# Kernel optimization log

Hardware: AMD Instinct MI355X
Metric: run time of the kernel (lower is better)

## Reference

```python
import jax, jax.numpy as jnp
import numpy as np

N_NODES = 50000
N_EDGES = 800000
IN_DIM = 128
HEADS1, D1 = 4, 16   # hidden_dim // 4 = 16, concat -> 64
HID = HEADS1 * D1    # 64
OUT_DIM = 40
NEG_SLOPE = 0.2      # PyG GATConv default


def setup_inputs() -> dict:
    key = jax.random.key(0)
    ks = jax.random.split(key, 11)
    x = jax.random.normal(ks[0], (N_NODES, IN_DIM), dtype=jnp.float32)
    edge_index = jax.random.randint(ks[1], (2, N_EDGES), 0, N_NODES)
    s1 = 1.0 / np.sqrt(IN_DIM)
    s2 = 1.0 / np.sqrt(HID)
    return {
        "x": x,
        "edge_index": edge_index,
        "W1": jax.random.normal(ks[2], (IN_DIM, HEADS1 * D1), dtype=jnp.float32) * s1,
        "a_src1": jax.random.normal(ks[3], (HEADS1, D1), dtype=jnp.float32) * s2,
        "a_dst1": jax.random.normal(ks[4], (HEADS1, D1), dtype=jnp.float32) * s2,
        "b1": jnp.zeros((HID,), dtype=jnp.float32),
        "W2": jax.random.normal(ks[5], (HID, OUT_DIM), dtype=jnp.float32) * s2,
        "a_src2": jax.random.normal(ks[6], (1, OUT_DIM), dtype=jnp.float32) * s2,
        "a_dst2": jax.random.normal(ks[7], (1, OUT_DIM), dtype=jnp.float32) * s2,
        "b2": jnp.zeros((OUT_DIM,), dtype=jnp.float32),
    }


def gat_conv(x, src, dst, W, a_src, a_dst, b, heads, d, n_nodes):
    # linear projection, split into heads: [N, H, d]
    h = (x @ W).reshape(n_nodes, heads, d)
    # per-node attention logits: [N, H]
    alpha_src = jnp.einsum("nhd,hd->nh", h, a_src)
    alpha_dst = jnp.einsum("nhd,hd->nh", h, a_dst)
    # edge attention coefficients
    e = jax.nn.leaky_relu(alpha_src[src] + alpha_dst[dst], NEG_SLOPE)  # [E, H]
    # segment softmax over incoming edges of each destination node
    e_max = jax.ops.segment_max(e, dst, num_segments=n_nodes)
    e_max = jnp.where(jnp.isfinite(e_max), e_max, 0.0)
    e_exp = jnp.exp(e - e_max[dst])
    denom = jax.ops.segment_sum(e_exp, dst, num_segments=n_nodes)
    alpha = e_exp / (denom[dst] + 1e-16)  # [E, H]
    # weighted scatter-aggregate of source messages
    out = jax.ops.segment_sum(h[src] * alpha[..., None], dst, num_segments=n_nodes)
    return out.reshape(n_nodes, heads * d) + b


def reference(x, edge_index, W1, a_src1, a_dst1, b1, W2, a_src2, a_dst2, b2):
    n = x.shape[0]
    # PyG GATConv add_self_loops=True
    loop = jnp.arange(n, dtype=edge_index.dtype)
    src = jnp.concatenate([edge_index[0], loop])
    dst = jnp.concatenate([edge_index[1], loop])
    h = jax.nn.relu(gat_conv(x, src, dst, W1, a_src1, a_dst1, b1, HEADS1, D1, n))
    # dropout is identity in eval mode
    h = gat_conv(h, src, dst, W2, a_src2, a_dst2, b2, 1, OUT_DIM, n)
    return jax.nn.log_softmax(h, axis=1)
```

## Files before the change

### kernel.cpp

```cpp
#include <hip/hip_runtime.h>
#include <hip/hip_fp16.h>
#include <math.h>

#define NN    50000
#define NE0   800000
#define NE    850000
#define INDIM 128
#define HID   64
#define OUTD  40

#define NB    391
#define BSH   7
#define BCAP  3072

typedef unsigned short u16;

__global__ __launch_bounds__(256) void k_bin(const int* __restrict__ ei,
                                             int* __restrict__ bcur,
                                             unsigned int* __restrict__ epack) {
    __shared__ int lh[NB];
    __shared__ int lbase[NB];
    __shared__ unsigned ebuf[3328];
    const int tid = threadIdx.x;
    const int CH = (NE + 255) / 256;
    const int e0 = blockIdx.x * CH;
    const int e1 = (e0 + CH < NE) ? e0 + CH : NE;
    const int cnt = e1 - e0;

    for (int i = tid; i < NB; i += 256) lh[i] = 0;
    __syncthreads();
    for (int i = tid; i < cnt; i += 256) {
        int e = e0 + i;
        int src, dst;
        if (e < NE0) { src = ei[e]; dst = ei[NE0 + e]; }
        else         { src = e - NE0; dst = src; }
        int bkt = dst >> BSH;
        ebuf[i] = (unsigned)src | ((unsigned)(dst & 127) << 16) | ((unsigned)bkt << 23);
        atomicAdd(&lh[bkt], 1);
    }
    __syncthreads();
    for (int i = tid; i < NB; i += 256) {
        int c = lh[i];
        lbase[i] = c ? atomicAdd(&bcur[i], c) : 0;
        lh[i] = 0;
    }
    __syncthreads();
    for (int i = tid; i < cnt; i += 256) {
        unsigned rec = ebuf[i];
        int bkt = rec >> 23;
        int lpos = atomicAdd(&lh[bkt], 1);
        epack[lbase[bkt] + lpos] = rec & 0x7FFFFFu;
    }
}

__global__ __launch_bounds__(256) void k_bucket_csr(
    const int* __restrict__ bcur, const unsigned int* __restrict__ epack,
    int* __restrict__ off_s, int* __restrict__ off_e, int* __restrict__ esrc) {
    __shared__ int lh[128];
    __shared__ int lcur[128];
    __shared__ int sblk;
    const int tid = threadIdx.x, lane = tid & 63;
    const int b = blockIdx.x;
    const int e0 = b * BCAP;
    const int cnt = bcur[b] - e0;

    if (tid < 128) lh[tid] = 0;
    __syncthreads();
    for (int i = tid; i < cnt; i += 256)
        atomicAdd(&lh[epack[e0 + i] >> 16], 1);
    __syncthreads();

    int v = 0, incl = 0;
    if (tid < 128) {
        v = lh[tid];
        incl = v;
#pragma unroll
        for (int s = 1; s < 64; s <<= 1) {
            int t = __shfl_up(incl, s);
            if (lane >= s) incl += t;
        }
    }
    if (tid == 63) sblk = incl;
    __syncthreads();
    if (tid >= 64 && tid < 128) incl += sblk;
    if (tid < 128) {
        int ex = e0 + incl - v;
        lcur[tid] = ex;
        int gd = b * 128 + tid;
        if (gd < NN) { off_s[gd] = ex; off_e[gd] = ex + v; }
    }
    __syncthreads();

    for (int i = tid; i < cnt; i += 256) {
        unsigned int p = epack[e0 + i];
        int pos = atomicAdd(&lcur[p >> 16], 1);
        esrc[pos] = (int)(p & 0xFFFFu);
    }
}

__global__ __launch_bounds__(256, 2) void k_gemm1(
    const float* __restrict__ x, const float* __restrict__ W1,
    const float* __restrict__ a_s, const float* __restrict__ a_d,
    __half* __restrict__ h1h, float* __restrict__ asrc1, float* __restrict__ adst1,
    int* __restrict__ bcur)
{
    __shared__ float Wl[INDIM * HID];
    __shared__ float xs[64 * 132];
    const int tid = threadIdx.x;
    const int r0 = blockIdx.x * 64;

    if (blockIdx.x == 0) {
        for (int i = tid; i < NB; i += 256) bcur[i] = i * BCAP;
    }

    const float4* W4 = (const float4*)W1;
    float4* Wl4 = (float4*)Wl;
#pragma unroll
    for (int i = 0; i < 8; ++i) Wl4[tid + i * 256] = W4[tid + i * 256];

    const float4* x4 = (const float4*)x;
#pragma unroll
    for (int i = 0; i < 8; ++i) {
        int idx = tid + i * 256;
        int row = idx >> 5;
        int k4  = idx & 31;
        int nr = r0 + row;
        float4 v = make_float4(0.f, 0.f, 0.f, 0.f);
        if (nr < NN) v = x4[(size_t)nr * 32 + k4];
        *(float4*)&xs[row * 132 + k4 * 4] = v;
    }
    __syncthreads();

    const int rg = tid >> 4;
    const int cg = tid & 15;
    const int c4 = cg * 4;
    const float as0 = a_s[c4], as1v = a_s[c4+1], as2v = a_s[c4+2], as3v = a_s[c4+3];
    const float ad0 = a_d[c4], ad1v = a_d[c4+1], ad2v = a_d[c4+2], ad3v = a_d[c4+3];

    float acc[4][4];
#pragma unroll
    for (int i = 0; i < 4; ++i)
#pragma unroll
        for (int j = 0; j < 4; ++j) acc[i][j] = 0.f;

#pragma unroll 4
    for (int k4 = 0; k4 < 32; ++k4) {
        float4 xv[4];
#pragma unroll
        for (int i = 0; i < 4; ++i)
            xv[i] = *(const float4*)&xs[(rg * 4 + i) * 132 + k4 * 4];
        const float* wp = &Wl[(k4 * 4) * HID + c4];
        float4 w0 = *(const float4*)(wp);
        float4 w1 = *(const float4*)(wp + HID);
        float4 w2 = *(const float4*)(wp + 2 * HID);
        float4 w3 = *(const float4*)(wp + 3 * HID);
#pragma unroll
        for (int i = 0; i < 4; ++i) {
            acc[i][0] += xv[i].x * w0.x + xv[i].y * w1.x + xv[i].z * w2.x + xv[i].w * w3.x;
            acc[i][1] += xv[i].x * w0.y + xv[i].y * w1.y + xv[i].z * w2.y + xv[i].w * w3.y;
            acc[i][2] += xv[i].x * w0.z + xv[i].y * w1.z + xv[i].z * w2.z + xv[i].w * w3.z;
            acc[i][3] += xv[i].x * w0.w + xv[i].y * w1.w + xv[i].z * w2.w + xv[i].w * w3.w;
        }
    }

#pragma unroll
    for (int i = 0; i < 4; ++i) {
        const int n = r0 + rg * 4 + i;
        if (n < NN) {
            __half2 ha = __floats2half2_rn(acc[i][0], acc[i][1]);
            __half2 hb = __floats2half2_rn(acc[i][2], acc[i][3]);
            *(__half2*)&h1h[(size_t)n * HID + c4]     = ha;
            *(__half2*)&h1h[(size_t)n * HID + c4 + 2] = hb;
        }
        float ps = acc[i][0] * as0 + acc[i][1] * as1v + acc[i][2] * as2v + acc[i][3] * as3v;
        float pd = acc[i][0] * ad0 + acc[i][1] * ad1v + acc[i][2] * ad2v + acc[i][3] * ad3v;
        ps += __shfl_xor(ps, 1); ps += __shfl_xor(ps, 2);
        pd += __shfl_xor(pd, 1); pd += __shfl_xor(pd, 2);
        if ((cg & 3) == 0 && n < NN) {
            int head = cg >> 2;
            asrc1[n * 4 + head] = ps;
            adst1[n * 4 + head] = pd;
        }
    }
}

__global__ __launch_bounds__(256) void k_fagg1(
    const int* __restrict__ off_s, const int* __restrict__ off_e,
    const int* __restrict__ esrc, const float* __restrict__ asrc1,
    const float* __restrict__ adst1,
    const __half* __restrict__ h1h, const float* __restrict__ b1,
    __half* __restrict__ hmid)
{
    const int wv = threadIdx.x >> 6, lane = threadIdx.x & 63;
    const int g = lane >> 4, li = lane & 15;
    const int n = blockIdx.x * 16 + wv * 4 + g;
    const int s0 = off_s[n], s1 = off_e[n];
    const int hp = li >> 2;
    const float adst = adst1[n * 4 + hp];
    const int last = s1 - 1;

    float l = 0.f, a0 = 0.f, a1 = 0.f, a2 = 0.f, a3 = 0.f;
    const char* hb = (const char*)h1h;
    for (int t = s0; t < s1; t += 8) {
        int sx[8];
        int ok[8];
#pragma unroll
        for (int j = 0; j < 8; ++j) {
            int ix  = t + j;
            ok[j] = (ix < s1);
            int ixc = ok[j] ? ix : last;
            sx[j] = esrc[ixc];
        }
        float ax[8];
#pragma unroll
        for (int j = 0; j < 8; ++j) ax[j] = asrc1[sx[j] * 4 + hp];
        float2 f0[8], f1[8];
#pragma unroll
        for (int j = 0; j < 8; ++j) {
            uint2 raw = *(const uint2*)(hb + ((size_t)sx[j] * 128 + li * 8));
            f0[j] = __half22float2(*(__half2*)&raw.x);
            f1[j] = __half22float2(*(__half2*)&raw.y);
        }
#pragma unroll
        for (int j = 0; j < 8; ++j) {
            float e = ax[j] + adst;
            e = (e > 0.f) ? e : 0.2f * e;
            float w = __expf(e);
            w = ok[j] ? w : 0.f;
            l  += w;
            a0 += w * f0[j].x;
            a1 += w * f0[j].y;
            a2 += w * f1[j].x;
            a3 += w * f1[j].y;
        }
    }
    float rcp = 1.f / l;
    float4 bv = *(const float4*)&b1[li * 4];
    float o0 = fmaxf(a0 * rcp + bv.x, 0.f);
    float o1 = fmaxf(a1 * rcp + bv.y, 0.f);
    float o2 = fmaxf(a2 * rcp + bv.z, 0.f);
    float o3 = fmaxf(a3 * rcp + bv.w, 0.f);
    __half2 ha = __floats2half2_rn(o0, o1);
    __half2 hc = __floats2half2_rn(o2, o3);
    uint2 st;
    st.x = *(unsigned*)&ha;
    st.y = *(unsigned*)&hc;
    *(uint2*)((char*)hmid + ((size_t)n * 128 + li * 8)) = st;
}

__global__ __launch_bounds__(320) void k_gemm2(
    const __half* __restrict__ hin, const float* __restrict__ W2,
    const float* __restrict__ a_s, const float* __restrict__ a_d,
    __half* __restrict__ h2h, float* __restrict__ asrc2, float* __restrict__ adst2)
{
    __shared__ float Wl[HID * OUTD];
    __shared__ float xs[32 * 68];
    __shared__ float s_as[32], s_ad[32];
    const int tid = threadIdx.x;
    const int r0 = blockIdx.x * 32;

    const float4* W4 = (const float4*)W2;
    float4* Wl4 = (float4*)Wl;
    for (int i = tid; i < 640; i += 320) Wl4[i] = W4[i];
    const uint2* x4 = (const uint2*)hin;
    for (int i = tid; i < 512; i += 320) {
        int row = i >> 4;
        int c   = i & 15;
        int nr = r0 + row;
        float4 v = make_float4(0.f, 0.f, 0.f, 0.f);
        if (nr < NN) {
            uint2 raw = x4[(size_t)nr * 16 + c];
            float2 p0 = __half22float2(*(__half2*)&raw.x);
            float2 p1 = __half22float2(*(__half2*)&raw.y);
            v = make_float4(p0.x, p0.y, p1.x, p1.y);
        }
        *(float4*)&xs[row * 68 + c * 4] = v;
    }
    if (tid < 32) { s_as[tid] = 0.f; s_ad[tid] = 0.f; }
    __syncthreads();

    const int r  = tid / 10;
    const int cg = tid % 10;
    const int c4 = cg * 4;
    float a0 = 0.f, a1 = 0.f, a2 = 0.f, a3 = 0.f;
#pragma unroll 4
    for (int k4 = 0; k4 < 16; ++k4) {
        float4 xv = *(const float4*)&xs[r * 68 + k4 * 4];
        const float* wp = &Wl[(k4 * 4) * OUTD + c4];
        float4 w0 = *(const float4*)(wp);
        float4 w1 = *(const float4*)(wp + OUTD);
        float4 w2 = *(const float4*)(wp + 2 * OUTD);
        float4 w3 = *(const float4*)(wp + 3 * OUTD);
        a0 += xv.x * w0.x + xv.y * w1.x + xv.z * w2.x + xv.w * w3.x;
        a1 += xv.x * w0.y + xv.y * w1.y + xv.z * w2.y + xv.w * w3.y;
        a2 += xv.x * w0.z + xv.y * w1.z + xv.z * w2.z + xv.w * w3.z;
        a3 += xv.x * w0.w + xv.y * w1.w + xv.z * w2.w + xv.w * w3.w;
    }
    const int n = r0 + r;
    float ps = a0 * a_s[c4] + a1 * a_s[c4 + 1] + a2 * a_s[c4 + 2] + a3 * a_s[c4 + 3];
    float pd = a0 * a_d[c4] + a1 * a_d[c4 + 1] + a2 * a_d[c4 + 2] + a3 * a_d[c4 + 3];
    atomicAdd(&s_as[r], ps);
    atomicAdd(&s_ad[r], pd);
    if (n < NN) {
        __half2 ha = __floats2half2_rn(a0, a1);
        __half2 hb = __floats2half2_rn(a2, a3);
        *(__half2*)&h2h[(size_t)n * OUTD + c4]     = ha;
        *(__half2*)&h2h[(size_t)n * OUTD + c4 + 2] = hb;
    }
    __syncthreads();
    if (tid < 32) {
        int n2 = r0 + tid;
        if (n2 < NN) { asrc2[n2] = s_as[tid]; adst2[n2] = s_ad[tid]; }
    }
}

__global__ __launch_bounds__(256) void k_fagg2(
    const int* __restrict__ off_s, const int* __restrict__ off_e,
    const int* __restrict__ esrc, const float* __restrict__ asrc2,
    const float* __restrict__ adst2,
    const __half* __restrict__ h2h, const float* __restrict__ b2,
    float* __restrict__ out)
{
    __shared__ float svals[24][OUTD];
    const int wv = threadIdx.x >> 6, lane = threadIdx.x & 63;
    const int g = lane / 10;
    const int li = lane - g * 10;
    const bool ga = (g < 6);
    const int n = blockIdx.x * 24 + wv * 6 + (ga ? g : 0);
    const bool valid = ga && (n < NN);
    const int s0 = valid ? off_s[n] : 0;
    const int s1 = valid ? off_e[n] : 0;
    const float adst = valid ? adst2[n] : 0.f;
    const int last = s1 - 1;

    float l = 0.f, a0 = 0.f, a1 = 0.f, a2 = 0.f, a3 = 0.f;
    const char* hb = (const char*)h2h;
    for (int t = s0; t < s1; t += 8) {
        int sx[8];
        int ok[8];
#pragma unroll
        for (int j = 0; j < 8; ++j) {
            int ix  = t + j;
            ok[j] = (ix < s1);
            int ixc = ok[j] ? ix : last;
            sx[j] = esrc[ixc];
        }
        float ax[8];
#pragma unroll
        for (int j = 0; j < 8; ++j) ax[j] = asrc2[sx[j]];
        float2 f0[8], f1[8];
#pragma unroll
        for (int j = 0; j < 8; ++j) {
            uint2 raw = *(const uint2*)(hb + ((size_t)sx[j] * 80 + li * 8));
            f0[j] = __half22float2(*(__half2*)&raw.x);
            f1[j] = __half22float2(*(__half2*)&raw.y);
        }
#pragma unroll
        for (int j = 0; j < 8; ++j) {
            float e = ax[j] + adst;
            e = (e > 0.f) ? e : 0.2f * e;
            float w = __expf(e);
            w = ok[j] ? w : 0.f;
            l  += w;
            a0 += w * f0[j].x;
            a1 += w * f0[j].y;
            a2 += w * f1[j].x;
            a3 += w * f1[j].y;
        }
    }
    if (valid) {
        float rcp = 1.f / l;
        float4 bv = *(const float4*)&b2[li * 4];
        int r = wv * 6 + g;
        svals[r][li * 4]     = a0 * rcp + bv.x;
        svals[r][li * 4 + 1] = a1 * rcp + bv.y;
        svals[r][li * 4 + 2] = a2 * rcp + bv.z;
        svals[r][li * 4 + 3] = a3 * rcp + bv.w;
    }
    __syncthreads();

    for (int r = wv; r < 24; r += 4) {
        int n2 = blockIdx.x * 24 + r;
        if (n2 >= NN) continue;
        float v = (lane < OUTD) ? svals[r][lane] : -1e30f;
        float mx = v;
#pragma unroll
        for (int o = 32; o; o >>= 1) mx = fmaxf(mx, __shfl_xor(mx, o));
        float ex = (lane < OUTD) ? __expf(v - mx) : 0.f;
        float sm = ex;
#pragma unroll
        for (int o = 32; o; o >>= 1) sm += __shfl_xor(sm, o);
        if (lane < OUTD) out[(size_t)n2 * OUTD + lane] = v - mx - __logf(sm);
    }
}

extern "C" void kernel_launch(void* const* d_in, const int* in_sizes, int n_in,
                              void* d_out, int out_size, void* d_ws, size_t ws_size,
                              hipStream_t stream)
{
    const float* x   = (const float*)d_in[0];
    const int*   ei  = (const int*)  d_in[1];
    const float* W1  = (const float*)d_in[2];
    const float* as1 = (const float*)d_in[3];
    const float* ad1 = (const float*)d_in[4];
    const float* b1  = (const float*)d_in[5];
    const float* W2  = (const float*)d_in[6];
    const float* as2 = (const float*)d_in[7];
    const float* ad2 = (const float*)d_in[8];
    const float* b2  = (const float*)d_in[9];
    float* out = (float*)d_out;

    char* ws = (char*)d_ws;
    __half* h1h   = (__half*)(ws);
    __half* hmidh = (__half*)(ws +  6400000);
    __half* h2h   = (__half*)(ws + 12800000);
    float*  asrc1 = (float*) (ws + 16800000);
    float*  adst1 = (float*) (ws + 17600000);
    float*  asrc2 = (float*) (ws + 18400000);
    float*  adst2 = (float*) (ws + 18600000);
    int*    off_s = (int*)   (ws + 18800000);
    int*    off_e = (int*)   (ws + 19000000);
    unsigned int* epack = (unsigned int*)(ws + 19200000);
    int*    esrc  = (int*)   (ws + 24004608);
    int*    bcur  = (int*)   (ws + 28809216);

    hipLaunchKernelGGL(k_gemm1,      dim3(782),  dim3(256), 0, stream, x, W1, as1, ad1, h1h, asrc1, adst1, bcur);
    hipLaunchKernelGGL(k_bin,        dim3(256),  dim3(256), 0, stream, ei, bcur, epack);
    hipLaunchKernelGGL(k_bucket_csr, dim3(NB),   dim3(256), 0, stream, bcur, epack, off_s, off_e, esrc);
    hipLaunchKernelGGL(k_fagg1,      dim3(3125), dim3(256), 0, stream, off_s, off_e, esrc, asrc1, adst1, h1h, b1, hmidh);
    hipLaunchKernelGGL(k_gemm2,      dim3(1563), dim3(320), 0, stream, hmidh, W2, as2, ad2, h2h, asrc2, adst2);
    hipLaunchKernelGGL(k_fagg2,      dim3(2084), dim3(256), 0, stream, off_s, off_e, esrc, asrc2, adst2, h2h, b2, out);
}
```

Measured before the change: 194.3 us.

## Fuse CSR build into GEMM1, fuse GEMM2 into layer-1 aggregation, prefetch edge indices

The bucket-to-CSR pass is merged into the layer-1 projection kernel, with the first NB blocks doing CSR work and the rest doing the GEMM, sharing LDS through a union. Layer-2 projection and its attention logits are computed inside the layer-1 aggregation kernel from the per-block results kept in LDS, so the intermediate hidden tensor is never written to or read from global memory. bcur is now zeroed with a memset and holds counts rather than offsets. Both aggregation loops software-pipeline the next batch of edge indices. This drops two launches and a round trip through global memory, but adds LDS pressure, a W2 load in every aggregation block, and a serialized GEMM phase at the end of aggregation.

Result: faster. 184.6 us (-5.0%).

```diff
diff --git a/kernel.cpp b/kernel.cpp
--- a/kernel.cpp
+++ b/kernel.cpp
@@ -12,8 +12,6 @@
 #define NB    391
 #define BSH   7
 #define BCAP  3072
-
-typedef unsigned short u16;
 
 __global__ __launch_bounds__(256) void k_bin(const int* __restrict__ ei,
                                              int* __restrict__ bcur,
@@ -41,7 +39,7 @@
     __syncthreads();
     for (int i = tid; i < NB; i += 256) {
         int c = lh[i];
-        lbase[i] = c ? atomicAdd(&bcur[i], c) : 0;
+        lbase[i] = c ? (i * BCAP + atomicAdd(&bcur[i], c)) : 0;
         lh[i] = 0;
     }
     __syncthreads();
@@ -53,68 +51,66 @@
     }
 }
 
-__global__ __launch_bounds__(256) void k_bucket_csr(
-    const int* __restrict__ bcur, const unsigned int* __restrict__ epack,
-    int* __restrict__ off_s, int* __restrict__ off_e, int* __restrict__ esrc) {
-    __shared__ int lh[128];
-    __shared__ int lcur[128];
-    __shared__ int sblk;
-    const int tid = threadIdx.x, lane = tid & 63;
-    const int b = blockIdx.x;
-    const int e0 = b * BCAP;
-    const int cnt = bcur[b] - e0;
-
-    if (tid < 128) lh[tid] = 0;
-    __syncthreads();
-    for (int i = tid; i < cnt; i += 256)
-        atomicAdd(&lh[epack[e0 + i] >> 16], 1);
-    __syncthreads();
-
-    int v = 0, incl = 0;
-    if (tid < 128) {
-        v = lh[tid];
-        incl = v;
-#pragma unroll
-        for (int s = 1; s < 64; s <<= 1) {
-            int t = __shfl_up(incl, s);
-            if (lane >= s) incl += t;
-        }
-    }
-    if (tid == 63) sblk = incl;
-    __syncthreads();
-    if (tid >= 64 && tid < 128) incl += sblk;
-    if (tid < 128) {
-        int ex = e0 + incl - v;
-        lcur[tid] = ex;
-        int gd = b * 128 + tid;
-        if (gd < NN) { off_s[gd] = ex; off_e[gd] = ex + v; }
-    }
-    __syncthreads();
-
-    for (int i = tid; i < cnt; i += 256) {
-        unsigned int p = epack[e0 + i];
-        int pos = atomicAdd(&lcur[p >> 16], 1);
-        esrc[pos] = (int)(p & 0xFFFFu);
-    }
-}
-
-__global__ __launch_bounds__(256, 2) void k_gemm1(
+union __align__(16) SMu {
+    struct { float Wl[INDIM * HID]; float xs[64 * 132]; } g;
+    struct { int lh[128]; int lcur[128]; int sblk; } c;
+};
+
+__global__ __launch_bounds__(256, 2) void k_g1csr(
     const float* __restrict__ x, const float* __restrict__ W1,
     const float* __restrict__ a_s, const float* __restrict__ a_d,
     __half* __restrict__ h1h, float* __restrict__ asrc1, float* __restrict__ adst1,
-    int* __restrict__ bcur)
+    const int* __restrict__ bcur, const unsigned int* __restrict__ epack,
+    int* __restrict__ off_s, int* __restrict__ off_e, int* __restrict__ esrc)
 {
-    __shared__ float Wl[INDIM * HID];
-    __shared__ float xs[64 * 132];
+    __shared__ SMu sm;
     const int tid = threadIdx.x;
-    const int r0 = blockIdx.x * 64;
-
-    if (blockIdx.x == 0) {
-        for (int i = tid; i < NB; i += 256) bcur[i] = i * BCAP;
-    }
+
+    if (blockIdx.x < NB) {
+        const int lane = tid & 63;
+        const int b = blockIdx.x;
+        const int e0 = b * BCAP;
+        const int cnt = bcur[b];
+
+        if (tid < 128) sm.c.lh[tid] = 0;
+        __syncthreads();
+        for (int i = tid; i < cnt; i += 256)
+            atomicAdd(&sm.c.lh[epack[e0 + i] >> 16], 1);
+        __syncthreads();
+
+        int v = 0, incl = 0;
+        if (tid < 128) {
+            v = sm.c.lh[tid];
+            incl = v;
+#pragma unroll
+            for (int s = 1; s < 64; s <<= 1) {
+                int t = __shfl_up(incl, s);
+                if (lane >= s) incl += t;
+            }
+        }
+        if (tid == 63) sm.c.sblk = incl;
+        __syncthreads();
+        if (tid >= 64 && tid < 128) incl += sm.c.sblk;
+        if (tid < 128) {
+            int ex = e0 + incl - v;
+            sm.c.lcur[tid] = ex;
+            int gd = b * 128 + tid;
+            if (gd < NN) { off_s[gd] = ex; off_e[gd] = ex + v; }
+        }
+        __syncthreads();
+
+        for (int i = tid; i < cnt; i += 256) {
+            unsigned int p = epack[e0 + i];
+            int pos = atomicAdd(&sm.c.lcur[p >> 16], 1);
+            esrc[pos] = (int)(p & 0xFFFFu);
+        }
+        return;
+    }
+
+    const int r0 = (blockIdx.x - NB) * 64;
 
     const float4* W4 = (const float4*)W1;
-    float4* Wl4 = (float4*)Wl;
+    float4* Wl4 = (float4*)sm.g.Wl;
 #pragma unroll
     for (int i = 0; i < 8; ++i) Wl4[tid + i * 256] = W4[tid + i * 256];
 
@@ -127,7 +123,7 @@
         int nr = r0 + row;
         float4 v = make_float4(0.f, 0.f, 0.f, 0.f);
         if (nr < NN) v = x4[(size_t)nr * 32 + k4];
-        *(float4*)&xs[row * 132 + k4 * 4] = v;
+        *(float4*)&sm.g.xs[row * 132 + k4 * 4] = v;
     }
     __syncthreads();
 
@@ -148,8 +144,8 @@
         float4 xv[4];
 #pragma unroll
         for (int i = 0; i < 4; ++i)
-            xv[i] = *(const float4*)&xs[(rg * 4 + i) * 132 + k4 * 4];
-        const float* wp = &Wl[(k4 * 4) * HID + c4];
+            xv[i] = *(const float4*)&sm.g.xs[(rg * 4 + i) * 132 + k4 * 4];
+        const float* wp = &sm.g.Wl[(k4 * 4) * HID + c4];
         float4 w0 = *(const float4*)(wp);
         float4 w1 = *(const float4*)(wp + HID);
         float4 w2 = *(const float4*)(wp + 2 * HID);
@@ -184,133 +180,125 @@
     }
 }
 
-__global__ __launch_bounds__(256) void k_fagg1(
+__global__ __launch_bounds__(256) void k_fagg1g2(
     const int* __restrict__ off_s, const int* __restrict__ off_e,
     const int* __restrict__ esrc, const float* __restrict__ asrc1,
     const float* __restrict__ adst1,
     const __half* __restrict__ h1h, const float* __restrict__ b1,
-    __half* __restrict__ hmid)
+    const float* __restrict__ W2, const float* __restrict__ a_s2,
+    const float* __restrict__ a_d2,
+    __half* __restrict__ h2h, float* __restrict__ asrc2, float* __restrict__ adst2)
 {
-    const int wv = threadIdx.x >> 6, lane = threadIdx.x & 63;
+    __shared__ __align__(16) float W2l[HID * OUTD];
+    __shared__ __align__(16) float hml[16][72];
+    __shared__ float s_a2s[OUTD], s_a2d[OUTD];
+    __shared__ float s_ps[16], s_pd[16];
+    const int tid = threadIdx.x;
+
+    {
+        const float4* W24 = (const float4*)W2;
+        float4* W2l4 = (float4*)W2l;
+        for (int i = tid; i < (HID * OUTD) / 4; i += 256) W2l4[i] = W24[i];
+        if (tid < OUTD) { s_a2s[tid] = a_s2[tid]; s_a2d[tid] = a_d2[tid]; }
+        if (tid < 16)   { s_ps[tid] = 0.f; s_pd[tid] = 0.f; }
+    }
+
+    const int wv = tid >> 6, lane = tid & 63;
     const int g = lane >> 4, li = lane & 15;
-    const int n = blockIdx.x * 16 + wv * 4 + g;
+    const int r = wv * 4 + g;
+    const int n = blockIdx.x * 16 + r;
     const int s0 = off_s[n], s1 = off_e[n];
     const int hp = li >> 2;
     const float adst = adst1[n * 4 + hp];
-    const int last = s1 - 1;
+    const int last = (s1 > 0) ? s1 - 1 : 0;
 
     float l = 0.f, a0 = 0.f, a1 = 0.f, a2 = 0.f, a3 = 0.f;
     const char* hb = (const char*)h1h;
+
+    int sxA[8];
+#pragma unroll
+    for (int j = 0; j < 8; ++j) {
+        int ix = s0 + j;
+        sxA[j] = esrc[ix < s1 ? ix : last];
+    }
     for (int t = s0; t < s1; t += 8) {
-        int sx[8];
-        int ok[8];
+        float ax[8];
+#pragma unroll
+        for (int j = 0; j < 8; ++j) ax[j] = asrc1[sxA[j] * 4 + hp];
+        uint2 raw[8];
+#pragma unroll
+        for (int j = 0; j < 8; ++j)
+            raw[j] = *(const uint2*)(hb + ((size_t)sxA[j] * 128 + li * 8));
+        int sxB[8];
+        const int t2 = t + 8;
 #pragma unroll
         for (int j = 0; j < 8; ++j) {
-            int ix  = t + j;
-            ok[j] = (ix < s1);
-            int ixc = ok[j] ? ix : last;
-            sx[j] = esrc[ixc];
-        }
-        float ax[8];
-#pragma unroll
-        for (int j = 0; j < 8; ++j) ax[j] = asrc1[sx[j] * 4 + hp];
-        float2 f0[8], f1[8];
-#pragma unroll
-        for (int j = 0; j < 8; ++j) {
-            uint2 raw = *(const uint2*)(hb + ((size_t)sx[j] * 128 + li * 8));
-            f0[j] = __half22float2(*(__half2*)&raw.x);
-            f1[j] = __half22float2(*(__half2*)&raw.y);
+            int ix = t2 + j;
+            sxB[j] = esrc[ix < s1 ? ix : last];
         }
 #pragma unroll
         for (int j = 0; j < 8; ++j) {
             float e = ax[j] + adst;
             e = (e > 0.f) ? e : 0.2f * e;
             float w = __expf(e);
-            w = ok[j] ? w : 0.f;
+            w = ((t + j) < s1) ? w : 0.f;
+            float2 f0 = __half22float2(*(__half2*)&raw[j].x);
+            float2 f1 = __half22float2(*(__half2*)&raw[j].y);
             l  += w;
-            a0 += w * f0[j].x;
-            a1 += w * f0[j].y;
-            a2 += w * f1[j].x;
-            a3 += w * f1[j].y;
-        }
-    }
-    float rcp = 1.f / l;
-    float4 bv = *(const float4*)&b1[li * 4];
-    float o0 = fmaxf(a0 * rcp + bv.x, 0.f);
-    float o1 = fmaxf(a1 * rcp + bv.y, 0.f);
-    float o2 = fmaxf(a2 * rcp + bv.z, 0.f);
-    float o3 = fmaxf(a3 * rcp + bv.w, 0.f);
-    __half2 ha = __floats2half2_rn(o0, o1);
-    __half2 hc = __floats2half2_rn(o2, o3);
-    uint2 st;
-    st.x = *(unsigned*)&ha;
-    st.y = *(unsigned*)&hc;
-    *(uint2*)((char*)hmid + ((size_t)n * 128 + li * 8)) = st;
-}
-
-__global__ __launch_bounds__(320) void k_gemm2(
-    const __half* __restrict__ hin, const float* __restrict__ W2,
-    const float* __restrict__ a_s, const float* __restrict__ a_d,
-    __half* __restrict__ h2h, float* __restrict__ asrc2, float* __restrict__ adst2)
-{
-    __shared__ float Wl[HID * OUTD];
-    __shared__ float xs[32 * 68];
-    __shared__ float s_as[32], s_ad[32];
-    const int tid = threadIdx.x;
-    const int r0 = blockIdx.x * 32;
-
-    const float4* W4 = (const float4*)W2;
-    float4* Wl4 = (float4*)Wl;
-    for (int i = tid; i < 640; i += 320) Wl4[i] = W4[i];
-    const uint2* x4 = (const uint2*)hin;
-    for (int i = tid; i < 512; i += 320) {
-        int row = i >> 4;
-        int c   = i & 15;
-        int nr = r0 + row;
-        float4 v = make_float4(0.f, 0.f, 0.f, 0.f);
-        if (nr < NN) {
-            uint2 raw = x4[(size_t)nr * 16 + c];
-            float2 p0 = __half22float2(*(__half2*)&raw.x);
-            float2 p1 = __half22float2(*(__half2*)&raw.y);
-            v = make_float4(p0.x, p0.y, p1.x, p1.y);
-        }
-        *(float4*)&xs[row * 68 + c * 4] = v;
-    }
-    if (tid < 32) { s_as[tid] = 0.f; s_ad[tid] = 0.f; }
-    __syncthreads();
-
-    const int r  = tid / 10;
-    const int cg = tid % 10;
-    const int c4 = cg * 4;
-    float a0 = 0.f, a1 = 0.f, a2 = 0.f, a3 = 0.f;
+            a0 += w * f0.x;
+            a1 += w * f0.y;
+            a2 += w * f1.x;
+            a3 += w * f1.y;
+        }
+#pragma unroll
+        for (int j = 0; j < 8; ++j) sxA[j] = sxB[j];
+    }
+
+    {
+        float rcp = 1.f / l;
+        float4 bv = *(const float4*)&b1[li * 4];
+        float o0 = fmaxf(a0 * rcp + bv.x, 0.f);
+        float o1 = fmaxf(a1 * rcp + bv.y, 0.f);
+        float o2 = fmaxf(a2 * rcp + bv.z, 0.f);
+        float o3 = fmaxf(a3 * rcp + bv.w, 0.f);
+        *(float4*)&hml[r][li * 4] = make_float4(o0, o1, o2, o3);
+    }
+    __syncthreads();
+
+    if (tid < 160) {
+        const int rr = tid / 10;
+        const int c4 = (tid - rr * 10) * 4;
+        float4 acc = make_float4(0.f, 0.f, 0.f, 0.f);
 #pragma unroll 4
-    for (int k4 = 0; k4 < 16; ++k4) {
-        float4 xv = *(const float4*)&xs[r * 68 + k4 * 4];
-        const float* wp = &Wl[(k4 * 4) * OUTD + c4];
-        float4 w0 = *(const float4*)(wp);
-        float4 w1 = *(const float4*)(wp + OUTD);
-        float4 w2 = *(const float4*)(wp + 2 * OUTD);
-        float4 w3 = *(const float4*)(wp + 3 * OUTD);
-        a0 += xv.x * w0.x + xv.y * w1.x + xv.z * w2.x + xv.w * w3.x;
-        a1 += xv.x * w0.y + xv.y * w1.y + xv.z * w2.y + xv.w * w3.y;
-        a2 += xv.x * w0.z + xv.y * w1.z + xv.z * w2.z + xv.w * w3.z;
-        a3 += xv.x * w0.w + xv.y * w1.w + xv.z * w2.w + xv.w * w3.w;
-    }
-    const int n = r0 + r;
-    float ps = a0 * a_s[c4] + a1 * a_s[c4 + 1] + a2 * a_s[c4 + 2] + a3 * a_s[c4 + 3];
-    float pd = a0 * a_d[c4] + a1 * a_d[c4 + 1] + a2 * a_d[c4 + 2] + a3 * a_d[c4 + 3];
-    atomicAdd(&s_as[r], ps);
-    atomicAdd(&s_ad[r], pd);
-    if (n < NN) {
-        __half2 ha = __floats2half2_rn(a0, a1);
-        __half2 hb = __floats2half2_rn(a2, a3);
-        *(__half2*)&h2h[(size_t)n * OUTD + c4]     = ha;
-        *(__half2*)&h2h[(size_t)n * OUTD + c4 + 2] = hb;
-    }
-    __syncthreads();
-    if (tid < 32) {
-        int n2 = r0 + tid;
-        if (n2 < NN) { asrc2[n2] = s_as[tid]; adst2[n2] = s_ad[tid]; }
+        for (int k4 = 0; k4 < 16; ++k4) {
+            float4 hv = *(const float4*)&hml[rr][k4 * 4];
+            const float* wp = &W2l[(k4 * 4) * OUTD + c4];
+            float4 w0 = *(const float4*)(wp);
+            float4 w1 = *(const float4*)(wp + OUTD);
+            float4 w2 = *(const float4*)(wp + 2 * OUTD);
+            float4 w3 = *(const float4*)(wp + 3 * OUTD);
+            acc.x += hv.x * w0.x + hv.y * w1.x + hv.z * w2.x + hv.w * w3.x;
+            acc.y += hv.x * w0.y + hv.y * w1.y + hv.z * w2.y + hv.w * w3.y;
+            acc.z += hv.x * w0.z + hv.y * w1.z + hv.z * w2.z + hv.w * w3.z;
+            acc.w += hv.x * w0.w + hv.y * w1.w + hv.z * w2.w + hv.w * w3.w;
+        }
+        const int n2 = blockIdx.x * 16 + rr;
+        __half2 ha = __floats2half2_rn(acc.x, acc.y);
+        __half2 hc = __floats2half2_rn(acc.z, acc.w);
+        uint2 st;
+        st.x = *(unsigned*)&ha;
+        st.y = *(unsigned*)&hc;
+        *(uint2*)((char*)h2h + ((size_t)n2 * 80 + c4 * 2)) = st;
+        float ps = acc.x * s_a2s[c4] + acc.y * s_a2s[c4 + 1] + acc.z * s_a2s[c4 + 2] + acc.w * s_a2s[c4 + 3];
+        float pd = acc.x * s_a2d[c4] + acc.y * s_a2d[c4 + 1] + acc.z * s_a2d[c4 + 2] + acc.w * s_a2d[c4 + 3];
+        atomicAdd(&s_ps[rr], ps);
+        atomicAdd(&s_pd[rr], pd);
+    }
+    __syncthreads();
+    if (tid < 16) {
+        const int n2 = blockIdx.x * 16 + tid;
+        asrc2[n2] = s_ps[tid];
+        adst2[n2] = s_pd[tid];
     }
 }
 
@@ -331,42 +319,48 @@
     const int s0 = valid ? off_s[n] : 0;
     const int s1 = valid ? off_e[n] : 0;
     const float adst = valid ? adst2[n] : 0.f;
-    const int last = s1 - 1;
+    const int last = (s1 > 0) ? s1 - 1 : 0;
 
     float l = 0.f, a0 = 0.f, a1 = 0.f, a2 = 0.f, a3 = 0.f;
     const char* hb = (const char*)h2h;
+
+    int sxA[8];
+#pragma unroll
+    for (int j = 0; j < 8; ++j) {
+        int ix = s0 + j;
+        sxA[j] = esrc[ix < s1 ? ix : last];
+    }
     for (int t = s0; t < s1; t += 8) {
-        int sx[8];
-        int ok[8];
+        float ax[8];
+#pragma unroll
+        for (int j = 0; j < 8; ++j) ax[j] = asrc2[sxA[j]];
+        uint2 raw[8];
+#pragma unroll
+        for (int j = 0; j < 8; ++j)
+            raw[j] = *(const uint2*)(hb + ((size_t)sxA[j] * 80 + li * 8));
+        int sxB[8];
+        const int t2 = t + 8;
 #pragma unroll
         for (int j = 0; j < 8; ++j) {
-            int ix  = t + j;
-            ok[j] = (ix < s1);
-            int ixc = ok[j] ? ix : last;
-            sx[j] = esrc[ixc];
-        }
-        float ax[8];
-#pragma unroll
-        for (int j = 0; j < 8; ++j) ax[j] = asrc2[sx[j]];
-        float2 f0[8], f1[8];
-#pragma unroll
-        for (int j = 0; j < 8; ++j) {
-            uint2 raw = *(const uint2*)(hb + ((size_t)sx[j] * 80 + li * 8));
-            f0[j] = __half22float2(*(__half2*)&raw.x);
-            f1[j] = __half22float2(*(__half2*)&raw.y);
+            int ix = t2 + j;
+            sxB[j] = esrc[ix < s1 ? ix : last];
         }
 #pragma unroll
         for (int j = 0; j < 8; ++j) {
             float e = ax[j] + adst;
             e = (e > 0.f) ? e : 0.2f * e;
             float w = __expf(e);
-            w = ok[j] ? w : 0.f;
+            w = ((t + j) < s1) ? w : 0.f;
+            float2 f0 = __half22float2(*(__half2*)&raw[j].x);
+            float2 f1 = __half22float2(*(__half2*)&raw[j].y);
             l  += w;
-            a0 += w * f0[j].x;
-            a1 += w * f0[j].y;
-            a2 += w * f1[j].x;
-            a3 += w * f1[j].y;
-        }
+            a0 += w * f0.x;
+            a1 += w * f0.y;
+            a2 += w * f1.x;
+            a3 += w * f1.y;
+        }
+#pragma unroll
+        for (int j = 0; j < 8; ++j) sxA[j] = sxB[j];
     }
     if (valid) {
         float rcp = 1.f / l;
@@ -412,7 +406,6 @@
 
     char* ws = (char*)d_ws;
     __half* h1h   = (__half*)(ws);
-    __half* hmidh = (__half*)(ws +  6400000);
     __half* h2h   = (__half*)(ws + 12800000);
     float*  asrc1 = (float*) (ws + 16800000);
     float*  adst1 = (float*) (ws + 17600000);
@@ -424,10 +417,12 @@
     int*    esrc  = (int*)   (ws + 24004608);
     int*    bcur  = (int*)   (ws + 28809216);
 
-    hipLaunchKernelGGL(k_gemm1,      dim3(782),  dim3(256), 0, stream, x, W1, as1, ad1, h1h, asrc1, adst1, bcur);
-    hipLaunchKernelGGL(k_bin,        dim3(256),  dim3(256), 0, stream, ei, bcur, epack);
-    hipLaunchKernelGGL(k_bucket_csr, dim3(NB),   dim3(256), 0, stream, bcur, epack, off_s, off_e, esrc);
-    hipLaunchKernelGGL(k_fagg1,      dim3(3125), dim3(256), 0, stream, off_s, off_e, esrc, asrc1, adst1, h1h, b1, hmidh);
-    hipLaunchKernelGGL(k_gemm2,      dim3(1563), dim3(320), 0, stream, hmidh, W2, as2, ad2, h2h, asrc2, adst2);
-    hipLaunchKernelGGL(k_fagg2,      dim3(2084), dim3(256), 0, stream, off_s, off_e, esrc, asrc2, adst2, h2h, b2, out);
+    hipMemsetAsync(bcur, 0, NB * sizeof(int), stream);
+    hipLaunchKernelGGL(k_bin,     dim3(256),      dim3(256), 0, stream, ei, bcur, epack);
+    hipLaunchKernelGGL(k_g1csr,   dim3(NB + 782), dim3(256), 0, stream,
+                       x, W1, as1, ad1, h1h, asrc1, adst1, bcur, epack, off_s, off_e, esrc);
+    hipLaunchKernelGGL(k_fagg1g2, dim3(3125),     dim3(256), 0, stream,
+                       off_s, off_e, esrc, asrc1, adst1, h1h, b1, W2, as2, ad2, h2h, asrc2, adst2);
+    hipLaunchKernelGGL(k_fagg2,   dim3(2084),     dim3(256), 0, stream,
+                       off_s, off_e, esrc, asrc2, adst2, h2h, b2, out);
 }
```
